# Performance work log

Measured on AMD Instinct MI355X. Metric: run time of the kernel, lower is better.

Reference implementation:

```python
import jax, jax.numpy as jnp
import numpy as np
from jax import lax

B = 65536

def _conv(x, w, b):
    y = lax.conv_general_dilated(x, w, (1, 1), 'VALID',
                                 dimension_numbers=('NCHW', 'OIHW', 'NCHW'))
    return y + b[None, :, None, None]

def _maxpool2(x):
    return lax.reduce_window(x, -jnp.inf, lax.max, (1, 1, 2, 2), (1, 1, 2, 2), 'VALID')

def _cnot01(s):  # control wire0, target wire1; s: [B,2,2] indexed [b,q0,q1]
    return jnp.stack([s[:, 0, :], s[:, 1, ::-1]], axis=1)

def _cnot10(s):  # control wire1, target wire0
    return jnp.stack([s[:, :, 0], s[:, ::-1, 1]], axis=2)

def _ry(half_angle):  # RY(2*half_angle) as used in circuit (theta/2 = half_angle)
    c, si = jnp.cos(half_angle), jnp.sin(half_angle)
    return jnp.stack([jnp.stack([c, -si]), jnp.stack([si, c])]).astype(jnp.complex64)

def _apply_w0(s, U):
    return jnp.einsum('ij,bjk->bik', U, s)

def _apply_w1(s, U):
    return jnp.einsum('ij,bkj->bki', U, s)

def _quantum(x2, p):
    # x2: [B,2] float32, p: [8] float32. Batched 2-qubit statevector sim.
    x0, x1 = x2[:, 0], x2[:, 1]
    n = x2.shape[0]
    s = jnp.full((n, 2, 2), 0.5 + 0.0j, dtype=jnp.complex64)  # H|0> x H|0>
    # RZ(2*x0) on wire 0: diag(e^{-i x0}, e^{i x0})
    s = s * jnp.exp(1j * jnp.stack([-x0, x0], axis=1).astype(jnp.complex64))[:, :, None]
    # RZ(2*x1) on wire 1
    s = s * jnp.exp(1j * jnp.stack([-x1, x1], axis=1).astype(jnp.complex64))[:, None, :]
    s = _cnot01(s)
    ang = (jnp.pi - x0) * (jnp.pi - x1)  # RZ(2*ang) on wire 1
    s = s * jnp.exp(1j * jnp.stack([-ang, ang], axis=1).astype(jnp.complex64))[:, None, :]
    s = _cnot01(s)
    s = _apply_w0(s, _ry(p[0])); s = _apply_w1(s, _ry(p[1])); s = _cnot01(s)
    s = _apply_w0(s, _ry(p[2])); s = _apply_w1(s, _ry(p[3])); s = _cnot10(s)
    s = _apply_w0(s, _ry(p[4])); s = _apply_w1(s, _ry(p[5])); s = _cnot01(s)
    s = _apply_w0(s, _ry(p[6])); s = _apply_w1(s, _ry(p[7]))
    z = jnp.array([[1.0, -1.0], [-1.0, 1.0]], dtype=jnp.float32)  # Z0 (x) Z1 signs
    prob = (s.real ** 2 + s.imag ** 2)
    return jnp.sum(prob * z[None], axis=(1, 2))  # [B]

def setup_inputs() -> dict:
    key = jax.random.key(0)
    ks = jax.random.split(key, 12)
    d = {}
    d['x'] = jax.random.normal(ks[0], (B, 1, 28, 28), dtype=jnp.float32)
    d['conv1_w'] = jax.random.normal(ks[1], (2, 1, 5, 5), dtype=jnp.float32) * 0.2
    d['conv1_b'] = jax.random.normal(ks[2], (2,), dtype=jnp.float32) * 0.1
    d['conv2_w'] = jax.random.normal(ks[3], (16, 2, 5, 5), dtype=jnp.float32) * 0.14
    d['conv2_b'] = jax.random.normal(ks[4], (16,), dtype=jnp.float32) * 0.1
    d['fc1_w'] = jax.random.normal(ks[5], (64, 256), dtype=jnp.float32) * 0.0625
    d['fc1_b'] = jax.random.normal(ks[6], (64,), dtype=jnp.float32) * 0.05
    d['fc2_w'] = jax.random.normal(ks[7], (2, 64), dtype=jnp.float32) * 0.125
    d['fc2_b'] = jax.random.normal(ks[8], (2,), dtype=jnp.float32) * 0.05
    d['fc3_w'] = jax.random.normal(ks[9], (1, 1), dtype=jnp.float32)
    d['fc3_b'] = jax.random.normal(ks[10], (1,), dtype=jnp.float32) * 0.05
    d['qnn_params'] = jax.random.uniform(ks[11], (8,), dtype=jnp.float32)
    return d

def reference(x, conv1_w, conv1_b, conv2_w, conv2_b, fc1_w, fc1_b,
              fc2_w, fc2_b, fc3_w, fc3_b, qnn_params):
    h = jax.nn.relu(_conv(x, conv1_w, conv1_b))        # [B,2,24,24]
    h = _maxpool2(h)                                    # [B,2,12,12]
    h = jax.nn.relu(_conv(h, conv2_w, conv2_b))        # [B,16,8,8]
    h = _maxpool2(h)                                    # [B,16,4,4]
    # Dropout2d: identity in eval mode
    h = h.reshape(h.shape[0], -1)                       # [B,256]
    h = jax.nn.relu(h @ fc1_w.T + fc1_b)                # [B,64]
    h = h @ fc2_w.T + fc2_b                             # [B,2]
    q = _quantum(h, qnn_params)[:, None]                # [B,1]
    y = q @ fc3_w.T + fc3_b                             # [B,1]
    logits = jnp.concatenate([y, 1.0 - y], axis=-1)     # [B,2]
    return jax.nn.log_softmax(logits, axis=1)
```

## Files before the change

### kernel.cpp

```cpp
#include <hip/hip_runtime.h>
#include <math.h>


typedef float v2f __attribute__((ext_vector_type(2)));
typedef float v4f __attribute__((ext_vector_type(4)));

static __device__ __forceinline__ v2f vfma2(v2f a, float w, v2f c) {
    return __builtin_elementwise_fma(a, (v2f){w, w}, c);
}
static __device__ __forceinline__ v2f vmax2(v2f a, v2f b) {
    return __builtin_elementwise_max(a, b);
}

#define P1_PAIR 580
#define HB_OC   36
#define HB_PAIR 576
#define W2_OC   60

__global__ __launch_bounds__(256, 5)
void hqcnn_fused(const float* __restrict__ x,
                 const float* __restrict__ w1,
                 const float* __restrict__ b1,
                 const float* __restrict__ w2,
                 const float* __restrict__ b2,
                 const float* __restrict__ fw1,
                 const float* __restrict__ fb1,
                 const float* __restrict__ fw2,
                 const float* __restrict__ fb2,
                 const float* __restrict__ fw3,
                 const float* __restrict__ fb3,
                 const float* __restrict__ qp,
                 float* __restrict__ out)
{
    __shared__ __align__(16) float p1s[4 * P1_PAIR];
    __shared__ __align__(16) float hb[4 * HB_PAIR];
    __shared__ __align__(16) float w2s[16 * W2_OC];

    const int t = threadIdx.x;
    const int wv = t >> 6;
    const int lane = t & 63;
    const long base = (long)blockIdx.x * 8;

    for (int f = t; f < 800; f += 256) {
        int oc = f / 50;
        int rem = f - oc * 50;
        int c = rem >= 25;
        int k = rem - c * 25;
        w2s[oc * W2_OC + c * 28 + k] = w2[f];
    }
    __syncthreads();

    {
        float w1c[50];
        #pragma unroll
        for (int i = 0; i < 50; ++i) w1c[i] = w1[i];
        const float bb0 = b1[0], bb1 = b1[1];
        const float* xA = x + (base + 2 * wv) * 784;
        const float* xB = xA + 784;

        for (int f = lane; f < 72; f += 64) {
            int i = f / 6, jh = f - i * 6;
            v2f acc[16];
            #pragma unroll
            for (int q = 0; q < 16; ++q) acc[q] = (v2f){0.f, 0.f};
            #pragma unroll
            for (int u = 0; u < 6; ++u) {
                const v4f* pA = (const v4f*)(xA + (2 * i + u) * 28 + 4 * jh);
                const v4f* pB = (const v4f*)(xB + (2 * i + u) * 28 + 4 * jh);
                v4f a0 = pA[0], a1 = pA[1];
                v4f b0 = pB[0], b1v = pB[1];
                v2f rr[8] = { {a0.x,b0.x},{a0.y,b0.y},{a0.z,b0.z},{a0.w,b0.w},
                              {a1.x,b1v.x},{a1.y,b1v.y},{a1.z,b1v.z},{a1.w,b1v.w} };
                #pragma unroll
                for (int a = 0; a < 2; ++a) {
                    if (a <= u && (u - a) <= 4) {
                        const int wu = u - a;
                        #pragma unroll
                        for (int c = 0; c < 2; ++c)
                            #pragma unroll
                            for (int b = 0; b < 4; ++b) {
                                v2f s0 = acc[c * 8 + a * 4 + b];
                                #pragma unroll
                                for (int v = 0; v < 5; ++v)
                                    s0 = vfma2(rr[b + v], w1c[c * 25 + wu * 5 + v], s0);
                                acc[c * 8 + a * 4 + b] = s0;
                            }
                    }
                }
            }
            #pragma unroll
            for (int c = 0; c < 2; ++c) {
                float bias = c ? bb1 : bb0;
                #pragma unroll
                for (int bb = 0; bb < 2; ++bb) {
                    v2f m = vmax2(vmax2(acc[c*8 + 2*bb],     acc[c*8 + 2*bb + 1]),
                                  vmax2(acc[c*8 + 4 + 2*bb], acc[c*8 + 4 + 2*bb + 1]));
                    m = m + (v2f){bias, bias};
                    m = vmax2(m, (v2f){0.f, 0.f});
                    ((v2f*)p1s)[wv * (P1_PAIR / 2) + c * 144 + i * 12 + 2 * jh + bb] = m;
                }
            }
        }
    }
    asm volatile("s_waitcnt lgkmcnt(0)" ::: "memory");

    {
        int oc = (lane >> 2) & 15;
        int qi = (lane >> 1) & 1;
        int qj = lane & 1;
        v2f acc[16];
        #pragma unroll
        for (int q = 0; q < 16; ++q) acc[q] = (v2f){0.f, 0.f};
        #pragma unroll
        for (int c = 0; c < 2; ++c) {
            float wvv[28];
            {
                const v4f* wp = (const v4f*)w2s + oc * (W2_OC / 4) + c * 7;
                #pragma unroll
                for (int j = 0; j < 7; ++j) {
                    v4f w4 = wp[j];
                    wvv[j*4+0] = w4.x; wvv[j*4+1] = w4.y; wvv[j*4+2] = w4.z; wvv[j*4+3] = w4.w;
                }
            }
            #pragma unroll
            for (int u = 0; u < 8; ++u) {
                int rb = wv * (P1_PAIR / 4) + c * 72 + (4 * qi + u) * 6 + 2 * qj;
                v4f q0 = ((const v4f*)p1s)[rb + 0];
                v4f q1 = ((const v4f*)p1s)[rb + 1];
                v4f q2 = ((const v4f*)p1s)[rb + 2];
                v4f q3 = ((const v4f*)p1s)[rb + 3];
                v2f rr[8] = { {q0.x,q0.y},{q0.z,q0.w},{q1.x,q1.y},{q1.z,q1.w},
                              {q2.x,q2.y},{q2.z,q2.w},{q3.x,q3.y},{q3.z,q3.w} };
                #pragma unroll
                for (int a = 0; a < 4; ++a) {
                    if (a <= u && (u - a) <= 4) {
                        const int wu = u - a;
                        #pragma unroll
                        for (int b = 0; b < 4; ++b) {
                            v2f s0 = acc[a * 4 + b];
                            #pragma unroll
                            for (int v = 0; v < 5; ++v)
                                s0 = vfma2(rr[b + v], wvv[wu * 5 + v], s0);
                            acc[a * 4 + b] = s0;
                        }
                    }
                }
            }
        }
        float bias = b2[oc];
        #pragma unroll
        for (int a2 = 0; a2 < 2; ++a2)
            #pragma unroll
            for (int b2i = 0; b2i < 2; ++b2i) {
                v2f m = vmax2(vmax2(acc[(2*a2)*4 + 2*b2i],     acc[(2*a2)*4 + 2*b2i + 1]),
                              vmax2(acc[(2*a2+1)*4 + 2*b2i], acc[(2*a2+1)*4 + 2*b2i + 1]));
                m = m + (v2f){bias, bias};
                m = vmax2(m, (v2f){0.f, 0.f});
                int pos = (2*qi + a2) * 4 + (2*qj + b2i);
                ((v2f*)hb)[wv * (HB_PAIR / 2) + oc * (HB_OC / 2) + pos] = m;
            }
    }
    __syncthreads();

    {
        const v4f* wrow = (const v4f*)(fw1 + lane * 256 + wv * 64);
        v2f part[4];
        #pragma unroll
        for (int p = 0; p < 4; ++p) part[p] = (v2f){0.f, 0.f};
        #pragma unroll
        for (int jo = 0; jo < 4; ++jo) {
            int oc = wv * 4 + jo;
            #pragma unroll
            for (int jj = 0; jj < 4; ++jj) {
                v4f w4 = wrow[jo * 4 + jj];
                #pragma unroll
                for (int p = 0; p < 4; ++p) {
                    const v4f* hp = (const v4f*)(hb + p * HB_PAIR + oc * HB_OC + jj * 8);
                    v4f hA = hp[0], hB = hp[1];
                    part[p] = vfma2((v2f){hA.x, hA.y}, w4.x, part[p]);
                    part[p] = vfma2((v2f){hA.z, hA.w}, w4.y, part[p]);
                    part[p] = vfma2((v2f){hB.x, hB.y}, w4.z, part[p]);
                    part[p] = vfma2((v2f){hB.z, hB.w}, w4.w, part[p]);
                }
            }
        }
        v2f* pb = (v2f*)p1s;
        #pragma unroll
        for (int p = 0; p < 4; ++p)
            pb[(wv * 4 + p) * 64 + lane] = part[p];
    }
    __syncthreads();

    {
        const v2f* pb = (const v2f*)p1s;
        float fb = fb1[lane];
        v2f acc = (v2f){fb, fb};
        acc = acc + pb[(0 * 4 + wv) * 64 + lane];
        acc = acc + pb[(1 * 4 + wv) * 64 + lane];
        acc = acc + pb[(2 * 4 + wv) * 64 + lane];
        acc = acc + pb[(3 * 4 + wv) * 64 + lane];
        v2f a2 = vmax2(acc, (v2f){0.f, 0.f});

        float w20 = fw2[lane], w21 = fw2[64 + lane];
        v2f pz0 = a2 * (v2f){w20, w20};
        v2f pz1 = a2 * (v2f){w21, w21};
        #pragma unroll
        for (int off = 32; off > 0; off >>= 1) {
            pz0.x += __shfl_xor(pz0.x, off, 64);
            pz0.y += __shfl_xor(pz0.y, off, 64);
            pz1.x += __shfl_xor(pz1.x, off, 64);
            pz1.y += __shfl_xor(pz1.y, off, 64);
        }
        int h = lane >> 5;
        float x0 = (h ? pz0.y : pz0.x) + fb2[0];
        float x1 = (h ? pz1.y : pz1.x) + fb2[1];

        float sr[4], si[4];
        {
            float th0 = -x0 - x1, th1 = -x0 + x1, th2 = x0 - x1, th3 = x0 + x1;
            sr[0] = 0.5f * __cosf(th0); si[0] = 0.5f * __sinf(th0);
            sr[1] = 0.5f * __cosf(th1); si[1] = 0.5f * __sinf(th1);
            sr[2] = 0.5f * __cosf(th2); si[2] = 0.5f * __sinf(th2);
            sr[3] = 0.5f * __cosf(th3); si[3] = 0.5f * __sinf(th3);
        }
        {
            float tr = sr[2]; sr[2] = sr[3]; sr[3] = tr;
            float ti = si[2]; si[2] = si[3]; si[3] = ti;
            float ang = ((float)M_PI - x0) * ((float)M_PI - x1);
            float ca = __cosf(ang), sa = __sinf(ang);
            float r, im;
            r = sr[0]; im = si[0]; sr[0] = r*ca + im*sa; si[0] = im*ca - r*sa;
            r = sr[2]; im = si[2]; sr[2] = r*ca + im*sa; si[2] = im*ca - r*sa;
            r = sr[1]; im = si[1]; sr[1] = r*ca - im*sa; si[1] = im*ca + r*sa;
            r = sr[3]; im = si[3]; sr[3] = r*ca - im*sa; si[3] = im*ca + r*sa;
            tr = sr[2]; sr[2] = sr[3]; sr[3] = tr;
            ti = si[2]; si[2] = si[3]; si[3] = ti;
        }
        float cp[8], sp[8];
        #pragma unroll
        for (int g = 0; g < 8; ++g) { float q = qp[g]; cp[g] = __cosf(q); sp[g] = __sinf(q); }

        #define QRY0(cc, ss) { \
            float a0r=sr[0], a0i=si[0], a1r=sr[2], a1i=si[2]; \
            sr[0]=cc*a0r-ss*a1r; si[0]=cc*a0i-ss*a1i; \
            sr[2]=ss*a0r+cc*a1r; si[2]=ss*a0i+cc*a1i; \
            float b0r=sr[1], b0i=si[1], b1r=sr[3], b1i=si[3]; \
            sr[1]=cc*b0r-ss*b1r; si[1]=cc*b0i-ss*b1i; \
            sr[3]=ss*b0r+cc*b1r; si[3]=ss*b0i+cc*b1i; }
        #define QRY1(cc, ss) { \
            float a0r=sr[0], a0i=si[0], a1r=sr[1], a1i=si[1]; \
            sr[0]=cc*a0r-ss*a1r; si[0]=cc*a0i-ss*a1i; \
            sr[1]=ss*a0r+cc*a1r; si[1]=ss*a0i+cc*a1i; \
            float b0r=sr[2], b0i=si[2], b1r=sr[3], b1i=si[3]; \
            sr[2]=cc*b0r-ss*b1r; si[2]=cc*b0i-ss*b1i; \
            sr[3]=ss*b0r+cc*b1r; si[3]=ss*b0i+cc*b1i; }
        #define QSWAP(i_, j_) { float tr=sr[i_]; sr[i_]=sr[j_]; sr[j_]=tr; \
                                float ti=si[i_]; si[i_]=si[j_]; si[j_]=ti; }

        QRY0(cp[0], sp[0]);
        QRY1(cp[1], sp[1]);
        QSWAP(2, 3);
        QRY0(cp[2], sp[2]);
        QRY1(cp[3], sp[3]);
        QSWAP(1, 3);
        QRY0(cp[4], sp[4]);
        QRY1(cp[5], sp[5]);
        QSWAP(2, 3);
        QRY0(cp[6], sp[6]);
        QRY1(cp[7], sp[7]);

        float qv = (sr[0]*sr[0] + si[0]*si[0])
                 - (sr[1]*sr[1] + si[1]*si[1])
                 - (sr[2]*sr[2] + si[2]*si[2])
                 + (sr[3]*sr[3] + si[3]*si[3]);
        float y = fmaf(qv, fw3[0], fb3[0]);
        float l0 = y, l1 = 1.0f - y;
        float m = fmaxf(l0, l1);
        float lse = m + __logf(__expf(l0 - m) + __expf(l1 - m));
        int lk = lane & 31;
        if (lk < 2) {
            float o = (lk == 0) ? (l0 - lse) : (l1 - lse);
            out[(base + 2 * wv + h) * 2 + lk] = o;
        }
        #undef QRY0
        #undef QRY1
        #undef QSWAP
    }
}

extern "C" void kernel_launch(void* const* d_in, const int* in_sizes, int n_in,
                              void* d_out, int out_size, void* d_ws, size_t ws_size,
                              hipStream_t stream) {
    const float* x   = (const float*)d_in[0];
    const float* w1  = (const float*)d_in[1];
    const float* b1  = (const float*)d_in[2];
    const float* w2  = (const float*)d_in[3];
    const float* b2  = (const float*)d_in[4];
    const float* fw1 = (const float*)d_in[5];
    const float* fb1 = (const float*)d_in[6];
    const float* fw2 = (const float*)d_in[7];
    const float* fb2 = (const float*)d_in[8];
    const float* fw3 = (const float*)d_in[9];
    const float* fb3 = (const float*)d_in[10];
    const float* qp  = (const float*)d_in[11];
    float* outp = (float*)d_out;

    int B = in_sizes[0] / 784;
    int nblk = B / 8;
    hipLaunchKernelGGL(hqcnn_fused, dim3(nblk), dim3(256), 0, stream,
                       x, w1, b1, w2, b2, fw1, fb1, fw2, fb2, fw3, fb3, qp, outp);
}
```

Before: 450.8 us.

## Pack conv1 output channels into packed FMA lanes with inline asm op_sel

Conv1 used to pack two samples into each v2f lane pair and run 72 work items per wave with 4-wide output strips. It now packs the two output channels into the v2f, with each item handling one sample and a 6-wide strip. Inline v_pk_fma_f32 with op_sel takes the broadcast input element from either half of a loaded float pair, so no repacking is needed. This cuts register shuffles and raises the per-wave item count to 96, using more lanes in the second pass. In exchange, pooled stores become scalar and interleaved by sample, and weights are forced into SGPR operands.

```diff
diff --git a/kernel.cpp b/kernel.cpp
--- a/kernel.cpp
+++ b/kernel.cpp
@@ -11,6 +11,13 @@
 static __device__ __forceinline__ v2f vmax2(v2f a, v2f b) {
     return __builtin_elementwise_max(a, b);
 }
+
+#define PK_FMA_W0(acc, w, xp) \
+    asm("v_pk_fma_f32 %0, %1, %2, %0 op_sel:[0,0,0] op_sel_hi:[1,0,1]" \
+        : "+v"(acc) : "s"(w), "v"(xp))
+#define PK_FMA_W1(acc, w, xp) \
+    asm("v_pk_fma_f32 %0, %1, %2, %0 op_sel:[0,1,0] op_sel_hi:[1,1,1]" \
+        : "+v"(acc) : "s"(w), "v"(xp))
 
 #define P1_PAIR 580
 #define HB_OC   36
@@ -51,53 +58,53 @@
     __syncthreads();
 
     {
-        float w1c[50];
-        #pragma unroll
-        for (int i = 0; i < 50; ++i) w1c[i] = w1[i];
-        const float bb0 = b1[0], bb1 = b1[1];
-        const float* xA = x + (base + 2 * wv) * 784;
-        const float* xB = xA + 784;
-
-        for (int f = lane; f < 72; f += 64) {
-            int i = f / 6, jh = f - i * 6;
-            v2f acc[16];
-            #pragma unroll
-            for (int q = 0; q < 16; ++q) acc[q] = (v2f){0.f, 0.f};
-            #pragma unroll
-            for (int u = 0; u < 6; ++u) {
-                const v4f* pA = (const v4f*)(xA + (2 * i + u) * 28 + 4 * jh);
-                const v4f* pB = (const v4f*)(xB + (2 * i + u) * 28 + 4 * jh);
-                v4f a0 = pA[0], a1 = pA[1];
-                v4f b0 = pB[0], b1v = pB[1];
-                v2f rr[8] = { {a0.x,b0.x},{a0.y,b0.y},{a0.z,b0.z},{a0.w,b0.w},
-                              {a1.x,b1v.x},{a1.y,b1v.y},{a1.z,b1v.z},{a1.w,b1v.w} };
-                #pragma unroll
-                for (int a = 0; a < 2; ++a) {
-                    if (a <= u && (u - a) <= 4) {
-                        const int wu = u - a;
-                        #pragma unroll
-                        for (int c = 0; c < 2; ++c)
+        v2f w1p[25];
+        #pragma unroll
+        for (int k = 0; k < 25; ++k)
+            w1p[k] = (v2f){w1[k], w1[25 + k]};
+        const v2f bias1 = (v2f){b1[0], b1[1]};
+
+        #pragma unroll
+        for (int it = 0; it < 2; ++it) {
+            int f = lane + it * 64;
+            if (f < 96) {
+                int s = f / 48;
+                int r = f - s * 48;
+                int i = r >> 2, jh = r & 3;
+                const float* xrow = x + (base + 2 * wv + s) * 784;
+                v2f acc[12];
+                #pragma unroll
+                for (int q = 0; q < 12; ++q) acc[q] = (v2f){0.f, 0.f};
+                #pragma unroll
+                for (int u = 0; u < 6; ++u) {
+                    const v2f* xp = (const v2f*)(xrow + (2 * i + u) * 28 + 6 * jh);
+                    v2f P[5] = { xp[0], xp[1], xp[2], xp[3], xp[4] };
+                    #pragma unroll
+                    for (int a = 0; a < 2; ++a) {
+                        if (a <= u && (u - a) <= 4) {
+                            const int wu = u - a;
                             #pragma unroll
-                            for (int b = 0; b < 4; ++b) {
-                                v2f s0 = acc[c * 8 + a * 4 + b];
+                            for (int v = 0; v < 5; ++v) {
                                 #pragma unroll
-                                for (int v = 0; v < 5; ++v)
-                                    s0 = vfma2(rr[b + v], w1c[c * 25 + wu * 5 + v], s0);
-                                acc[c * 8 + a * 4 + b] = s0;
+                                for (int j = 0; j < 6; ++j) {
+                                    const int e = j + v;
+                                    if (e & 1) { PK_FMA_W1(acc[a * 6 + j], w1p[wu * 5 + v], P[e >> 1]); }
+                                    else       { PK_FMA_W0(acc[a * 6 + j], w1p[wu * 5 + v], P[e >> 1]); }
+                                }
                             }
+                        }
                     }
                 }
-            }
-            #pragma unroll
-            for (int c = 0; c < 2; ++c) {
-                float bias = c ? bb1 : bb0;
-                #pragma unroll
-                for (int bb = 0; bb < 2; ++bb) {
-                    v2f m = vmax2(vmax2(acc[c*8 + 2*bb],     acc[c*8 + 2*bb + 1]),
-                                  vmax2(acc[c*8 + 4 + 2*bb], acc[c*8 + 4 + 2*bb + 1]));
-                    m = m + (v2f){bias, bias};
-                    m = vmax2(m, (v2f){0.f, 0.f});
-                    ((v2f*)p1s)[wv * (P1_PAIR / 2) + c * 144 + i * 12 + 2 * jh + bb] = m;
+                #pragma unroll
+                for (int m = 0; m < 3; ++m) {
+                    v2f mx = vmax2(vmax2(acc[2 * m], acc[2 * m + 1]),
+                                   vmax2(acc[6 + 2 * m], acc[7 + 2 * m]));
+                    mx = mx + bias1;
+                    mx = vmax2(mx, (v2f){0.f, 0.f});
+                    int pc = 3 * jh + m;
+                    int off = wv * P1_PAIR + 2 * (i * 12 + pc) + s;
+                    p1s[off] = mx.x;
+                    p1s[off + 288] = mx.y;
                 }
             }
         }
```

Measured after the change: 413.6 us. -8.3%, faster.
